# Optimization experiments

Measured on AMD Instinct MI355X. Metric: run time of the kernel, lower is better.

The kernel has to match this reference:

```python
import jax, jax.numpy as jnp
import numpy as np

N, T, D, H = 2, 2048, 1024, 16
DH = D // H  # per-head dim = 64


def setup_inputs() -> dict:
    key = jax.random.key(0)
    k1, k2, k3, k4 = jax.random.split(key, 4)
    x = jax.random.normal(k1, (N, T, D), dtype=jnp.float32)
    W = jax.random.normal(k2, (D, 3 * D), dtype=jnp.float32) * (D ** -0.5)
    proj_w = jax.random.normal(k3, (D, D), dtype=jnp.float32) * (D ** -0.5)
    proj_b = jax.random.normal(k4, (D,), dtype=jnp.float32) * 0.02
    return {"x": x, "W": W, "proj_w": proj_w, "proj_b": proj_b}


def reference(x, W, proj_w, proj_b):
    n, t, d = x.shape
    qkv = x @ W                                   # [N,T,3D]
    q, k, v = jnp.split(qkv, 3, axis=-1)          # each [N,T,D]
    def heads(a):
        return a.reshape(n, t, H, DH).transpose(0, 2, 1, 3)  # [N,H,T,DH]
    q, k, v = heads(q), heads(k), heads(v)
    scale = DH ** -0.5
    scores = jnp.einsum('nhtd,nhsd->nhts', q, k) * scale      # [N,H,T,T]
    causal = jnp.tril(jnp.ones((t, t), dtype=bool))
    scores = jnp.where(causal, scores, jnp.finfo(scores.dtype).min)
    w = jax.nn.softmax(scores, axis=-1)
    out = jnp.einsum('nhts,nhsd->nhtd', w, v)                 # [N,H,T,DH]
    out = out.transpose(0, 2, 1, 3).reshape(n, t, d)          # [N,T,D]
    return out @ proj_w.T + proj_b
```

## Files before the change

kernel.cpp:

```cpp
#include <hip/hip_runtime.h>
#include <hip/hip_bf16.h>
#include <stdint.h>

#define N_B 2
#define T_S 2048
#define D_M 1024
#define H_N 16
#define D_H 64

typedef __bf16 bf16_t;
typedef __bf16 bf16x8 __attribute__((ext_vector_type(8)));
typedef float f32x4 __attribute__((ext_vector_type(4)));
typedef float f32x16 __attribute__((ext_vector_type(16)));

__device__ __forceinline__ void async_ld16(const void* g, void* lds_uniform_base) {
  __builtin_amdgcn_global_load_lds(
      (const __attribute__((address_space(1))) uint32_t*)(uintptr_t)g,
      (__attribute__((address_space(3))) uint32_t*)(uintptr_t)lds_uniform_base,
      16, 0, 0);
}

__global__ __launch_bounds__(256) void cvt_kernel(const float* __restrict__ in,
                                                  bf16_t* __restrict__ out, int n4) {
  int i = blockIdx.x * blockDim.x + threadIdx.x;
  if (i < n4) {
    float4 v = ((const float4*)in)[i];
    union { bf16_t b[4]; uint64_t u; } o;
    o.b[0] = (bf16_t)v.x; o.b[1] = (bf16_t)v.y;
    o.b[2] = (bf16_t)v.z; o.b[3] = (bf16_t)v.w;
    *(uint64_t*)(out + (size_t)i * 4) = o.u;
  }
}

__global__ __launch_bounds__(256) void transpose_cvt_kernel(const float* __restrict__ in,
                                                            bf16_t* __restrict__ out,
                                                            int R, int C) {
  __shared__ float tile[32][33];
  int bx = blockIdx.x * 32;
  int by = blockIdx.y * 32;
  int tx = threadIdx.x, ty = threadIdx.y;
#pragma unroll
  for (int i = 0; i < 32; i += 8)
    tile[ty + i][tx] = in[(size_t)(by + ty + i) * C + bx + tx];
  __syncthreads();
#pragma unroll
  for (int i = 0; i < 32; i += 8)
    out[(size_t)(bx + ty + i) * R + by + tx] = (bf16_t)tile[tx][ty + i];
}

template <int MODE>
__global__ __launch_bounds__(256) void gemm_bt_kernel(
    const bf16_t* __restrict__ A, const bf16_t* __restrict__ Bt,
    bf16_t* __restrict__ Qo, bf16_t* __restrict__ Ko, bf16_t* __restrict__ Vto,
    const float* __restrict__ bias, float* __restrict__ Co,
    int nbx, int cpx) {
  __shared__ bf16_t As[128 * 32];
  __shared__ bf16_t Bs[128 * 32];
  const int tid = threadIdx.x;
  const int lane = tid & 63;
  const int wid = tid >> 6;
  const int wr = wid >> 1, wc = wid & 1;
  const int g = lane >> 4, lr = lane & 15;
  const int d_ = blockIdx.x;
  const int orig = (d_ & 7) * cpx + (d_ >> 3);
  const int brow = (orig / nbx) * 128;
  const int bcol = (orig % nbx) * 128;

  f32x4 acc[4][4] = {};

  for (int k0 = 0; k0 < 1024; k0 += 32) {
#pragma unroll
    for (int q = 0; q < 2; ++q) {
      int idx = wid * 128 + q * 64 + lane;
      int row = idx >> 2, part = (idx & 3) * 8;
      async_ld16(A + (size_t)(brow + row) * 1024 + k0 + part,
                 &As[(wid * 128 + q * 64) * 8]);
      async_ld16(Bt + (size_t)(bcol + row) * 1024 + k0 + part,
                 &Bs[(wid * 128 + q * 64) * 8]);
    }
    __syncthreads();
    bf16x8 af[4], bfr[4];
#pragma unroll
    for (int i = 0; i < 4; ++i) {
      af[i]  = *(const bf16x8*)&As[(wr * 64 + i * 16 + lr) * 32 + g * 8];
      bfr[i] = *(const bf16x8*)&Bs[(wc * 64 + i * 16 + lr) * 32 + g * 8];
    }
#pragma unroll
    for (int i = 0; i < 4; ++i)
#pragma unroll
      for (int j = 0; j < 4; ++j)
        acc[i][j] = __builtin_amdgcn_mfma_f32_16x16x32_bf16(af[i], bfr[j], acc[i][j], 0, 0, 0);
    __syncthreads();
  }

#pragma unroll
  for (int i = 0; i < 4; ++i) {
    int row0 = brow + wr * 64 + i * 16 + g * 4;
#pragma unroll
    for (int j = 0; j < 4; ++j) {
      int col = bcol + wc * 64 + j * 16 + lr;
#pragma unroll
      for (int r = 0; r < 4; ++r) {
        int row = row0 + r;
        float v = acc[i][j][r];
        if (MODE == 0) {
          int n = row >> 11, t = row & (T_S - 1);
          int which = col >> 10, d = col & (D_M - 1);
          int h = d >> 6, dh = d & 63;
          if (which == 0)
            Qo[((size_t)(n * H_N + h) * T_S + t) * D_H + dh] = (bf16_t)v;
          else if (which == 1)
            Ko[((size_t)(n * H_N + h) * T_S + t) * D_H + dh] = (bf16_t)v;
          else
            Vto[((size_t)(n * H_N + h) * D_H + dh) * T_S + t] = (bf16_t)v;
        } else {
          Co[(size_t)row * D_M + col] = v + bias[col];
        }
      }
    }
  }
}

__global__ __launch_bounds__(256, 4) void attn_kernel(const bf16_t* __restrict__ Q,
                                                      const bf16_t* __restrict__ K,
                                                      const bf16_t* __restrict__ Vt,
                                                      bf16_t* __restrict__ O) {
  __shared__ bf16_t Ks[2][4096];
  __shared__ bf16_t Vs[2][4096];
  __shared__ float Linv[64];

  const int tid = threadIdx.x;
  const int lane = tid & 63;
  const int w = tid >> 6;
  const int qsub = w >> 1, khalf = w & 1;
  const int l31 = lane & 31;
  const int hi = lane >> 5;

  const int d_ = blockIdx.x;
  const int x = d_ & 7;
  const int s = d_ >> 3;
  const int hs = s & 3, j_ = s >> 2;
  const int t_ = j_ >> 3, m_ = j_ & 7;
  const int qc = (t_ == 0) ? (31 - m_) : (t_ == 1) ? (16 + m_)
               : (t_ == 2) ? (15 - m_) : m_;
  const int nh = x * 4 + hs;
  const bf16_t* Qg = Q + (size_t)nh * T_S * D_H;
  const char* Kb = (const char*)(K + (size_t)nh * T_S * D_H);
  const char* Vb = (const char*)(Vt + (size_t)nh * D_H * T_S);
  const int n = nh >> 4, h = nh & 15;

  const int c0 = (w * 2 + 0) * 64 + lane;
  const int c1 = (w * 2 + 1) * 64 + lane;
  const int r0_ = c0 >> 3, cb0 = (c0 & 7) * 16, sw0 = (r0_ & 7) << 4;
  const int r1_ = c1 >> 3, cb1 = (c1 & 7) * 16, sw1 = (r1_ & 7) << 4;
  const int koff0 = r0_ * 128 + (cb0 ^ sw0), koff1 = r1_ * 128 + (cb1 ^ sw1);
  const int voff0 = r0_ * 4096 + (cb0 ^ sw0), voff1 = r1_ * 4096 + (cb1 ^ sw1);
  const int lds0 = (w * 2 + 0) * 1024, lds1 = (w * 2 + 1) * 1024;

  const int q0w = qc * 64 + qsub * 32;
  const int nt = qc + 1;

  bf16x8 qf[4];
#pragma unroll
  for (int ksd = 0; ksd < 4; ++ksd) {
    bf16x8 t = *(const bf16x8*)(Qg + (size_t)(q0w + l31) * D_H + ksd * 16 + hi * 8);
#pragma unroll
    for (int e = 0; e < 8; ++e) t[e] = (bf16_t)((float)t[e] * 0.125f);
    qf[ksd] = t;
  }

  const int kabs_ = khalf * 32 + l31;
  int kfo[4];
#pragma unroll
  for (int ksd = 0; ksd < 4; ++ksd)
    kfo[ksd] = (kabs_ * 128 + ksd * 32 + hi * 16) ^ ((kabs_ & 7) << 4);
  int vfo[2][2];
#pragma unroll
  for (int db = 0; db < 2; ++db)
#pragma unroll
    for (int kk = 0; kk < 2; ++kk) {
      int dd = db * 32 + l31;
      vfo[db][kk] = (dd * 128 + khalf * 64 + kk * 32 + hi * 16) ^ ((dd & 7) << 4);
    }

  f32x16 oacc[2] = {};
  float lsum = 0.f;

  auto issue = [&](int t, int b) {
    const char* kt_ = Kb + (size_t)t * 8192;
    const char* vt_ = Vb + (size_t)t * 128;
    async_ld16(kt_ + koff0, (char*)Ks[b] + lds0);
    async_ld16(kt_ + koff1, (char*)Ks[b] + lds1);
    async_ld16(vt_ + voff0, (char*)Vs[b] + lds0);
    async_ld16(vt_ + voff1, (char*)Vs[b] + lds1);
  };

  auto compute = [&](int kt, int b, bool domask) {
    f32x16 S = {};
    __builtin_amdgcn_s_setprio(1);
#pragma unroll
    for (int ksd = 0; ksd < 4; ++ksd) {
      bf16x8 kf = *(const bf16x8*)((char*)Ks[b] + kfo[ksd]);
      S = __builtin_amdgcn_mfma_f32_32x32x16_bf16(kf, qf[ksd], S, 0, 0, 0);
    }
    __builtin_amdgcn_s_setprio(0);

    if (domask) {
#pragma unroll
      for (int r = 0; r < 16; ++r) {
        int ktile = khalf * 32 + (r & 3) + 8 * (r >> 2) + 4 * hi;
        if (kt * 64 + ktile > q0w + l31) S[r] = -1.0e30f;
      }
    }

    float p[16];
#pragma unroll
    for (int r = 0; r < 16; ++r) {
      p[r] = __builtin_amdgcn_exp2f(fminf(S[r] * 1.442695041f, 50.f));
      lsum += p[r];
    }

    uint32_t dw[8];
#pragma unroll
    for (int i = 0; i < 8; ++i) {
      union { bf16_t b2[2]; uint32_t u; } pk;
      pk.b2[0] = (bf16_t)p[2 * i];
      pk.b2[1] = (bf16_t)p[2 * i + 1];
      dw[i] = pk.u;
    }

    bf16x8 pa[2];
#pragma unroll
    for (int kk = 0; kk < 2; ++kk) {
      uint32_t u0 = dw[kk * 4 + 0], u1 = dw[kk * 4 + 1];
      uint32_t u2 = dw[kk * 4 + 2], u3 = dw[kk * 4 + 3];
      uint32_t sa = __shfl_xor(hi ? u0 : u2, 32, 64);
      uint32_t sb = __shfl_xor(hi ? u1 : u3, 32, 64);
      union { uint32_t u[4]; bf16x8 v; } f;
      f.u[0] = hi ? sa : u0;
      f.u[1] = hi ? sb : u1;
      f.u[2] = hi ? u2 : sa;
      f.u[3] = hi ? u3 : sb;
      pa[kk] = f.v;
    }

    __builtin_amdgcn_s_setprio(1);
#pragma unroll
    for (int db = 0; db < 2; ++db)
#pragma unroll
      for (int kk = 0; kk < 2; ++kk) {
        bf16x8 vf = *(const bf16x8*)((char*)Vs[b] + vfo[db][kk]);
        oacc[db] = __builtin_amdgcn_mfma_f32_32x32x16_bf16(pa[kk], vf, oacc[db], 0, 0, 0);
      }
    __builtin_amdgcn_s_setprio(0);
  };

  issue(0, 0);
  int buf = 0;
  for (int kt = 0; kt < nt; ++kt) {
    asm volatile("s_waitcnt vmcnt(0)" ::: "memory");
    __builtin_amdgcn_s_barrier();
    __builtin_amdgcn_sched_barrier(0);
    if (kt + 1 < nt) issue(kt + 1, buf ^ 1);
    compute(kt, buf, kt == nt - 1);
    buf ^= 1;
  }

  lsum += __shfl_xor(lsum, 32, 64);

  __syncthreads();
  float* mO = (float*)Ks;
  float* mL = (float*)Vs;
  if (khalf == 1) {
    float* ob = mO + qsub * 2048;
#pragma unroll
    for (int db = 0; db < 2; ++db)
#pragma unroll
      for (int r = 0; r < 16; ++r)
        ob[(db * 16 + r) * 64 + lane] = oacc[db][r];
    mL[qsub * 32 + l31] = lsum;
  }
  __syncthreads();
  if (khalf == 0) {
    float* ob = mO + qsub * 2048;
    float ltot = lsum + mL[qsub * 32 + l31];
    Linv[qsub * 32 + l31] = 1.f / ltot;
#pragma unroll
    for (int db = 0; db < 2; ++db)
#pragma unroll
      for (int r = 0; r < 16; ++r)
        oacc[db][r] += ob[(db * 16 + r) * 64 + lane];
#pragma unroll
    for (int r = 0; r < 16; ++r) {
      int ro = (r & 3) + 8 * (r >> 2) + 4 * hi;
      int qrow = q0w + ro;
      float inv = Linv[qsub * 32 + ro];
#pragma unroll
      for (int db = 0; db < 2; ++db)
        O[(size_t)(n * T_S + qrow) * D_M + h * D_H + db * 32 + l31] =
            (bf16_t)(oacc[db][r] * inv);
    }
  }
}

extern "C" void kernel_launch(void* const* d_in, const int* in_sizes, int n_in,
                              void* d_out, int out_size, void* d_ws, size_t ws_size,
                              hipStream_t stream) {
  const float* x  = (const float*)d_in[0];
  const float* W  = (const float*)d_in[1];
  const float* pw = (const float*)d_in[2];
  const float* pb = (const float*)d_in[3];
  float* out = (float*)d_out;

  char* ws = (char*)d_ws;
  bf16_t* x_bf = (bf16_t*)(ws);
  bf16_t* Wt   = (bf16_t*)(ws + (8ull  << 20));
  bf16_t* pwb  = (bf16_t*)(ws + (14ull << 20));
  bf16_t* Qh   = (bf16_t*)(ws + (16ull << 20));
  bf16_t* Kh   = (bf16_t*)(ws + (24ull << 20));
  bf16_t* Vth  = (bf16_t*)(ws + (32ull << 20));
  bf16_t* Oa   = (bf16_t*)(ws + (40ull << 20));

  cvt_kernel<<<4096, 256, 0, stream>>>(x, x_bf, (4096 * 1024) / 4);
  transpose_cvt_kernel<<<dim3(96, 32), dim3(32, 8), 0, stream>>>(W, Wt, 1024, 3072);
  cvt_kernel<<<1024, 256, 0, stream>>>(pw, pwb, (1024 * 1024) / 4);

  gemm_bt_kernel<0><<<768, 256, 0, stream>>>(x_bf, Wt, Qh, Kh, Vth, nullptr, nullptr, 24, 96);

  attn_kernel<<<1024, 256, 0, stream>>>(Qh, Kh, Vth, Oa);

  gemm_bt_kernel<1><<<256, 256, 0, stream>>>(Oa, pwb, nullptr, nullptr, nullptr, pb, out, 8, 32);
}
```

Before: 109.7 us.

## Replace QKV projection GEMM with 256x256-tile double-buffered async-LDS kernel

Adds a dedicated QKV GEMM kernel with 512 threads and 256x256 output tiles per block. Each K-slice is streamed into a swizzled LDS double buffer through global_load_lds, so the next slice loads while MFMA 16x16x32 instructions consume the current one. The bigger tiles are meant to raise operand reuse and cut global traffic compared with the generic templated GEMM. In exchange the grid shrinks to 192 blocks, which leaves some CUs idle, and the kernel uses a large LDS footprint.

```diff
diff --git a/kernel.cpp b/kernel.cpp
--- a/kernel.cpp
+++ b/kernel.cpp
@@ -121,6 +121,109 @@
   }
 }
 
+__global__ __launch_bounds__(512, 2) void gemm_qkv8_kernel(
+    const bf16_t* __restrict__ A, const bf16_t* __restrict__ Bt,
+    bf16_t* __restrict__ Qo, bf16_t* __restrict__ Ko, bf16_t* __restrict__ Vto) {
+  __shared__ bf16_t lds8[65536];
+
+  const int tid = threadIdx.x;
+  const int lane = tid & 63;
+  const int wv = tid >> 6;
+  const int wm = wv >> 2;
+  const int wn = wv & 3;
+  const int lr = lane & 15, g = lane >> 4;
+  const int swz = (lr & 7) << 4;
+
+  const int d_ = blockIdx.x;
+  const int orig = (d_ & 7) * 24 + (d_ >> 3);
+  const int brow = (orig / 12) * 256;
+  const int bcol = (orig % 12) * 256;
+
+  f32x4 acc[8][4] = {};
+
+  auto stage = [&](int kt, int dbuf_) {
+    char* ldsb = (char*)lds8 + dbuf_ * 65536;
+#pragma unroll
+    for (int q = 0; q < 8; ++q) {
+      int ch = q * 512 + tid;
+      int sec = ch >> 10;
+      int cs = ch & 1023;
+      int r = cs >> 3, cb = (cs & 7) * 16;
+      int srcb = cb ^ ((r & 7) << 4);
+      const char* gsrc;
+      if (sec < 2)
+        gsrc = (const char*)A + (size_t)(brow + sec * 128 + r) * 2048 + kt * 128 + srcb;
+      else
+        gsrc = (const char*)Bt + (size_t)(bcol + (sec - 2) * 128 + r) * 2048 + kt * 128 + srcb;
+      async_ld16(gsrc, ldsb + (q * 512 + wv * 64) * 16);
+    }
+  };
+
+  stage(0, 0);
+  for (int t = 0; t < 16; ++t) {
+    const int db = t & 1;
+    if (t + 1 < 16) {
+      stage(t + 1, db ^ 1);
+      asm volatile("s_waitcnt vmcnt(8)" ::: "memory");
+    } else {
+      asm volatile("s_waitcnt vmcnt(0)" ::: "memory");
+    }
+    __builtin_amdgcn_s_barrier();
+    __builtin_amdgcn_sched_barrier(0);
+
+    const char* Abase = (const char*)lds8 + db * 65536 + wm * 16384;
+    const char* Bbase = (const char*)lds8 + db * 65536 + 32768 + (wn >> 1) * 16384 + (wn & 1) * 8192;
+
+#pragma unroll
+    for (int b = 0; b < 2; ++b) {
+      bf16x8 bfr[4];
+#pragma unroll
+      for (int nf = 0; nf < 4; ++nf)
+        bfr[nf] = *(const bf16x8*)(Bbase + ((nf * 2048 + lr * 128 + b * 64 + g * 16) ^ swz));
+#pragma unroll
+      for (int half = 0; half < 2; ++half) {
+        bf16x8 af[4];
+#pragma unroll
+        for (int i = 0; i < 4; ++i)
+          af[i] = *(const bf16x8*)(Abase + (((half * 4 + i) * 2048 + lr * 128 + b * 64 + g * 16) ^ swz));
+        __builtin_amdgcn_s_setprio(1);
+#pragma unroll
+        for (int i = 0; i < 4; ++i)
+#pragma unroll
+          for (int nf = 0; nf < 4; ++nf)
+            acc[half * 4 + i][nf] =
+                __builtin_amdgcn_mfma_f32_16x16x32_bf16(af[i], bfr[nf], acc[half * 4 + i][nf], 0, 0, 0);
+        __builtin_amdgcn_s_setprio(0);
+        asm volatile("s_waitcnt lgkmcnt(0)" ::: "memory");
+        __builtin_amdgcn_s_barrier();
+      }
+    }
+  }
+
+#pragma unroll
+  for (int mf = 0; mf < 8; ++mf) {
+    int row0 = brow + wm * 128 + mf * 16 + g * 4;
+#pragma unroll
+    for (int nf = 0; nf < 4; ++nf) {
+      int col = bcol + wn * 64 + nf * 16 + lr;
+      int which = col >> 10, dcol = col & (D_M - 1);
+      int hh = dcol >> 6, dh = dcol & 63;
+#pragma unroll
+      for (int r = 0; r < 4; ++r) {
+        int row = row0 + r;
+        int nn = row >> 11, tt = row & (T_S - 1);
+        float v = acc[mf][nf][r];
+        if (which == 0)
+          Qo[((size_t)(nn * H_N + hh) * T_S + tt) * D_H + dh] = (bf16_t)v;
+        else if (which == 1)
+          Ko[((size_t)(nn * H_N + hh) * T_S + tt) * D_H + dh] = (bf16_t)v;
+        else
+          Vto[((size_t)(nn * H_N + hh) * D_H + dh) * T_S + tt] = (bf16_t)v;
+      }
+    }
+  }
+}
+
 __global__ __launch_bounds__(256, 4) void attn_kernel(const bf16_t* __restrict__ Q,
                                                       const bf16_t* __restrict__ K,
                                                       const bf16_t* __restrict__ Vt,
@@ -325,7 +428,7 @@
   transpose_cvt_kernel<<<dim3(96, 32), dim3(32, 8), 0, stream>>>(W, Wt, 1024, 3072);
   cvt_kernel<<<1024, 256, 0, stream>>>(pw, pwb, (1024 * 1024) / 4);
 
-  gemm_bt_kernel<0><<<768, 256, 0, stream>>>(x_bf, Wt, Qh, Kh, Vth, nullptr, nullptr, 24, 96);
+  gemm_qkv8_kernel<<<192, 512, 0, stream>>>(x_bf, Wt, Qh, Kh, Vth);
 
   attn_kernel<<<1024, 256, 0, stream>>>(Qh, Kh, Vth, Oa);
 
```

Measured after the change: 128.0 us. 16.7% more time.

## Double-buffer GEMM K-loop with 64-wide tiles, XOR-swizzled LDS, and merged conversion launches

Applied to the files above, without the earlier changes.

Rewrites the GEMM main loop to take K in steps of 64 using a double-buffered 64KB LDS region. The next tile is prefetched with async global-to-LDS loads while MFMAs run on the current one, and an XOR swizzle on LDS addresses avoids bank conflicts. This targets the stall after each load-then-barrier step and halves the number of barriers. Separately, the two float-to-bf16 conversion kernels are merged into a single launch. The larger LDS footprint can lower occupancy, and the manual waitcnt counts must match the issued loads for correctness.

```diff
diff --git a/kernel.cpp b/kernel.cpp
--- a/kernel.cpp
+++ b/kernel.cpp
@@ -20,16 +20,19 @@
       16, 0, 0);
 }
 
-__global__ __launch_bounds__(256) void cvt_kernel(const float* __restrict__ in,
-                                                  bf16_t* __restrict__ out, int n4) {
+__global__ __launch_bounds__(256) void cvt2_kernel(const float* __restrict__ in1,
+                                                   bf16_t* __restrict__ out1, int n1,
+                                                   const float* __restrict__ in2,
+                                                   bf16_t* __restrict__ out2) {
   int i = blockIdx.x * blockDim.x + threadIdx.x;
-  if (i < n4) {
-    float4 v = ((const float4*)in)[i];
-    union { bf16_t b[4]; uint64_t u; } o;
-    o.b[0] = (bf16_t)v.x; o.b[1] = (bf16_t)v.y;
-    o.b[2] = (bf16_t)v.z; o.b[3] = (bf16_t)v.w;
-    *(uint64_t*)(out + (size_t)i * 4) = o.u;
-  }
+  const float* in = in1;
+  bf16_t* out = out1;
+  if (i >= n1) { i -= n1; in = in2; out = out2; }
+  float4 v = ((const float4*)in)[i];
+  union { bf16_t b[4]; uint64_t u; } o;
+  o.b[0] = (bf16_t)v.x; o.b[1] = (bf16_t)v.y;
+  o.b[2] = (bf16_t)v.z; o.b[3] = (bf16_t)v.w;
+  *(uint64_t*)(out + (size_t)i * 4) = o.u;
 }
 
 __global__ __launch_bounds__(256) void transpose_cvt_kernel(const float* __restrict__ in,
@@ -54,8 +57,7 @@
     bf16_t* __restrict__ Qo, bf16_t* __restrict__ Ko, bf16_t* __restrict__ Vto,
     const float* __restrict__ bias, float* __restrict__ Co,
     int nbx, int cpx) {
-  __shared__ bf16_t As[128 * 32];
-  __shared__ bf16_t Bs[128 * 32];
+  __shared__ bf16_t lds[32768];
   const int tid = threadIdx.x;
   const int lane = tid & 63;
   const int wid = tid >> 6;
@@ -68,29 +70,61 @@
 
   f32x4 acc[4][4] = {};
 
-  for (int k0 = 0; k0 < 1024; k0 += 32) {
-#pragma unroll
-    for (int q = 0; q < 2; ++q) {
-      int idx = wid * 128 + q * 64 + lane;
-      int row = idx >> 2, part = (idx & 3) * 8;
-      async_ld16(A + (size_t)(brow + row) * 1024 + k0 + part,
-                 &As[(wid * 128 + q * 64) * 8]);
-      async_ld16(Bt + (size_t)(bcol + row) * 1024 + k0 + part,
-                 &Bs[(wid * 128 + q * 64) * 8]);
-    }
-    __syncthreads();
-    bf16x8 af[4], bfr[4];
-#pragma unroll
-    for (int i = 0; i < 4; ++i) {
-      af[i]  = *(const bf16x8*)&As[(wr * 64 + i * 16 + lr) * 32 + g * 8];
-      bfr[i] = *(const bf16x8*)&Bs[(wc * 64 + i * 16 + lr) * 32 + g * 8];
-    }
-#pragma unroll
-    for (int i = 0; i < 4; ++i)
-#pragma unroll
-      for (int j = 0; j < 4; ++j)
-        acc[i][j] = __builtin_amdgcn_mfma_f32_16x16x32_bf16(af[i], bfr[j], acc[i][j], 0, 0, 0);
-    __syncthreads();
+  int srow[8], scb[8], sdst[8];
+#pragma unroll
+  for (int q = 0; q < 8; ++q) {
+    int c = q * 256 + tid;
+    int sec = c >> 10;
+    int cs = c & 1023;
+    int row = cs >> 3, col = cs & 7;
+    srow[q] = row;
+    scb[q] = (col * 16) ^ ((row & 7) << 4);
+    sdst[q] = sec * 16384 + cs * 16;
+  }
+
+  auto stage = [&](int t, int b) {
+    char* base = (char*)lds + b * 32768;
+#pragma unroll
+    for (int q = 0; q < 8; ++q) {
+      const char* gsrc = (q < 4)
+          ? (const char*)A + (size_t)(brow + srow[q]) * 2048 + t * 128 + scb[q]
+          : (const char*)Bt + (size_t)(bcol + srow[q]) * 2048 + t * 128 + scb[q];
+      async_ld16(gsrc, base + sdst[q]);
+    }
+  };
+
+  stage(0, 0);
+  for (int t = 0; t < 16; ++t) {
+    if (t + 1 < 16) {
+      stage(t + 1, (t + 1) & 1);
+      asm volatile("s_waitcnt vmcnt(8)" ::: "memory");
+    } else {
+      asm volatile("s_waitcnt vmcnt(0)" ::: "memory");
+    }
+    __builtin_amdgcn_s_barrier();
+    __builtin_amdgcn_sched_barrier(0);
+
+    const char* base = (const char*)lds + (t & 1) * 32768;
+#pragma unroll
+    for (int b = 0; b < 2; ++b) {
+      bf16x8 af[4], bfr[4];
+#pragma unroll
+      for (int i = 0; i < 4; ++i) {
+        int ra = wr * 64 + i * 16 + lr;
+        int rb = wc * 64 + i * 16 + lr;
+        af[i]  = *(const bf16x8*)(base + ra * 128 + ((b * 64 + g * 16) ^ ((ra & 7) << 4)));
+        bfr[i] = *(const bf16x8*)(base + 16384 + rb * 128 + ((b * 64 + g * 16) ^ ((rb & 7) << 4)));
+      }
+      __builtin_amdgcn_s_setprio(1);
+#pragma unroll
+      for (int i = 0; i < 4; ++i)
+#pragma unroll
+        for (int j = 0; j < 4; ++j)
+          acc[i][j] = __builtin_amdgcn_mfma_f32_16x16x32_bf16(af[i], bfr[j], acc[i][j], 0, 0, 0);
+      __builtin_amdgcn_s_setprio(0);
+    }
+    asm volatile("s_waitcnt lgkmcnt(0)" ::: "memory");
+    __builtin_amdgcn_s_barrier();
   }
 
 #pragma unroll
@@ -321,9 +355,8 @@
   bf16_t* Vth  = (bf16_t*)(ws + (32ull << 20));
   bf16_t* Oa   = (bf16_t*)(ws + (40ull << 20));
 
-  cvt_kernel<<<4096, 256, 0, stream>>>(x, x_bf, (4096 * 1024) / 4);
+  cvt2_kernel<<<5120, 256, 0, stream>>>(x, x_bf, (4096 * 1024) / 4, pw, pwb);
   transpose_cvt_kernel<<<dim3(96, 32), dim3(32, 8), 0, stream>>>(W, Wt, 1024, 3072);
-  cvt_kernel<<<1024, 256, 0, stream>>>(pw, pwb, (1024 * 1024) / 4);
 
   gemm_bt_kernel<0><<<768, 256, 0, stream>>>(x_bf, Wt, Qh, Kh, Vth, nullptr, nullptr, 24, 96);
 
```

Measured after the change: 112.5 us. +2.6%, slower.

## Double-buffer GEMM LDS loads and fuse input conversion kernels into one launch

Applied to the files above, without the earlier changes.

The GEMM main loop now uses two LDS buffers per operand, issuing the async global-to-LDS loads for the next k-tile before computing the current one. It waits with explicit vmcnt counts and raw barriers, and raises wave priority around the MFMA block. Separately, the three conversion/transpose kernels are merged into a single prep kernel that dispatches on block index, saving two launches. LDS use doubles per block, which may reduce occupancy, and the manual waitcnt logic must stay correct.

```diff
diff --git a/kernel.cpp b/kernel.cpp
--- a/kernel.cpp
+++ b/kernel.cpp
@@ -20,32 +20,36 @@
       16, 0, 0);
 }
 
-__global__ __launch_bounds__(256) void cvt_kernel(const float* __restrict__ in,
-                                                  bf16_t* __restrict__ out, int n4) {
-  int i = blockIdx.x * blockDim.x + threadIdx.x;
-  if (i < n4) {
+__global__ __launch_bounds__(256) void prep_kernel(
+    const float* __restrict__ x, bf16_t* __restrict__ x_bf,
+    const float* __restrict__ pw, bf16_t* __restrict__ pwb,
+    const float* __restrict__ W, bf16_t* __restrict__ Wt) {
+  __shared__ float tile[32][33];
+  const int bid = blockIdx.x;
+  if (bid < 5120) {
+    int i = bid * 256 + threadIdx.x;
+    const float* in = x;
+    bf16_t* out = x_bf;
+    const int n1 = (4096 * 1024) / 4;
+    if (i >= n1) { i -= n1; in = pw; out = pwb; }
     float4 v = ((const float4*)in)[i];
     union { bf16_t b[4]; uint64_t u; } o;
     o.b[0] = (bf16_t)v.x; o.b[1] = (bf16_t)v.y;
     o.b[2] = (bf16_t)v.z; o.b[3] = (bf16_t)v.w;
     *(uint64_t*)(out + (size_t)i * 4) = o.u;
-  }
-}
-
-__global__ __launch_bounds__(256) void transpose_cvt_kernel(const float* __restrict__ in,
-                                                            bf16_t* __restrict__ out,
-                                                            int R, int C) {
-  __shared__ float tile[32][33];
-  int bx = blockIdx.x * 32;
-  int by = blockIdx.y * 32;
-  int tx = threadIdx.x, ty = threadIdx.y;
-#pragma unroll
-  for (int i = 0; i < 32; i += 8)
-    tile[ty + i][tx] = in[(size_t)(by + ty + i) * C + bx + tx];
-  __syncthreads();
-#pragma unroll
-  for (int i = 0; i < 32; i += 8)
-    out[(size_t)(bx + ty + i) * R + by + tx] = (bf16_t)tile[tx][ty + i];
+  } else {
+    const int tb = bid - 5120;
+    const int bx = (tb % 96) * 32;
+    const int by = (tb / 96) * 32;
+    const int tx = threadIdx.x & 31, ty = threadIdx.x >> 5;
+#pragma unroll
+    for (int i = 0; i < 32; i += 8)
+      tile[ty + i][tx] = W[(size_t)(by + ty + i) * 3072 + bx + tx];
+    __syncthreads();
+#pragma unroll
+    for (int i = 0; i < 32; i += 8)
+      Wt[(size_t)(bx + ty + i) * 1024 + by + tx] = (bf16_t)tile[tx][ty + i];
+  }
 }
 
 template <int MODE>
@@ -54,8 +58,8 @@
     bf16_t* __restrict__ Qo, bf16_t* __restrict__ Ko, bf16_t* __restrict__ Vto,
     const float* __restrict__ bias, float* __restrict__ Co,
     int nbx, int cpx) {
-  __shared__ bf16_t As[128 * 32];
-  __shared__ bf16_t Bs[128 * 32];
+  __shared__ bf16_t As[2][4096];
+  __shared__ bf16_t Bs[2][4096];
   const int tid = threadIdx.x;
   const int lane = tid & 63;
   const int wid = tid >> 6;
@@ -68,40 +72,59 @@
 
   f32x4 acc[4][4] = {};
 
-  for (int k0 = 0; k0 < 1024; k0 += 32) {
-#pragma unroll
-    for (int q = 0; q < 2; ++q) {
-      int idx = wid * 128 + q * 64 + lane;
-      int row = idx >> 2, part = (idx & 3) * 8;
-      async_ld16(A + (size_t)(brow + row) * 1024 + k0 + part,
-                 &As[(wid * 128 + q * 64) * 8]);
-      async_ld16(Bt + (size_t)(bcol + row) * 1024 + k0 + part,
-                 &Bs[(wid * 128 + q * 64) * 8]);
-    }
-    __syncthreads();
+  const int idx0 = wid * 128 + lane;
+  const int idx1 = wid * 128 + 64 + lane;
+  const int row0 = idx0 >> 2, part0 = (idx0 & 3) * 8;
+  const int row1 = idx1 >> 2, part1 = (idx1 & 3) * 8;
+  const int dst0 = (wid * 128) * 8;
+  const int dst1 = (wid * 128 + 64) * 8;
+
+  auto stage = [&](int t, int b) {
+    async_ld16(A + (size_t)(brow + row0) * 1024 + t * 32 + part0, &As[b][dst0]);
+    async_ld16(Bt + (size_t)(bcol + row0) * 1024 + t * 32 + part0, &Bs[b][dst0]);
+    async_ld16(A + (size_t)(brow + row1) * 1024 + t * 32 + part1, &As[b][dst1]);
+    async_ld16(Bt + (size_t)(bcol + row1) * 1024 + t * 32 + part1, &Bs[b][dst1]);
+  };
+
+  stage(0, 0);
+  for (int t = 0; t < 32; ++t) {
+    if (t + 1 < 32) {
+      stage(t + 1, (t + 1) & 1);
+      asm volatile("s_waitcnt vmcnt(4)" ::: "memory");
+    } else {
+      asm volatile("s_waitcnt vmcnt(0)" ::: "memory");
+    }
+    __builtin_amdgcn_s_barrier();
+    __builtin_amdgcn_sched_barrier(0);
+
+    const bf16_t* as = As[t & 1];
+    const bf16_t* bs = Bs[t & 1];
     bf16x8 af[4], bfr[4];
 #pragma unroll
     for (int i = 0; i < 4; ++i) {
-      af[i]  = *(const bf16x8*)&As[(wr * 64 + i * 16 + lr) * 32 + g * 8];
-      bfr[i] = *(const bf16x8*)&Bs[(wc * 64 + i * 16 + lr) * 32 + g * 8];
-    }
+      af[i]  = *(const bf16x8*)&as[(wr * 64 + i * 16 + lr) * 32 + g * 8];
+      bfr[i] = *(const bf16x8*)&bs[(wc * 64 + i * 16 + lr) * 32 + g * 8];
+    }
+    __builtin_amdgcn_s_setprio(1);
 #pragma unroll
     for (int i = 0; i < 4; ++i)
 #pragma unroll
       for (int j = 0; j < 4; ++j)
         acc[i][j] = __builtin_amdgcn_mfma_f32_16x16x32_bf16(af[i], bfr[j], acc[i][j], 0, 0, 0);
-    __syncthreads();
+    __builtin_amdgcn_s_setprio(0);
+    asm volatile("s_waitcnt lgkmcnt(0)" ::: "memory");
+    __builtin_amdgcn_s_barrier();
   }
 
 #pragma unroll
   for (int i = 0; i < 4; ++i) {
-    int row0 = brow + wr * 64 + i * 16 + g * 4;
+    int row0_ = brow + wr * 64 + i * 16 + g * 4;
 #pragma unroll
     for (int j = 0; j < 4; ++j) {
       int col = bcol + wc * 64 + j * 16 + lr;
 #pragma unroll
       for (int r = 0; r < 4; ++r) {
-        int row = row0 + r;
+        int row = row0_ + r;
         float v = acc[i][j][r];
         if (MODE == 0) {
           int n = row >> 11, t = row & (T_S - 1);
@@ -321,9 +344,7 @@
   bf16_t* Vth  = (bf16_t*)(ws + (32ull << 20));
   bf16_t* Oa   = (bf16_t*)(ws + (40ull << 20));
 
-  cvt_kernel<<<4096, 256, 0, stream>>>(x, x_bf, (4096 * 1024) / 4);
-  transpose_cvt_kernel<<<dim3(96, 32), dim3(32, 8), 0, stream>>>(W, Wt, 1024, 3072);
-  cvt_kernel<<<1024, 256, 0, stream>>>(pw, pwb, (1024 * 1024) / 4);
+  prep_kernel<<<8192, 256, 0, stream>>>(x, x_bf, pw, pwb, W, Wt);
 
   gemm_bt_kernel<0><<<768, 256, 0, stream>>>(x_bf, Wt, Qh, Kh, Vth, nullptr, nullptr, 24, 96);
 
```

New measurement: 102.3 us. 6.8% less time.
